# Kernel optimization log

Hardware: AMD Instinct MI355X
Metric: run time of the kernel (lower is better)

## Reference

```python
import jax, jax.numpy as jnp
import numpy as np

N, S, D = 4, 2048, 1024
H, HD = 16, 64  # heads, head_dim = patch_size // heads
SCALE = 1.0 / np.float32(np.sqrt(D))  # module divides by sqrt(patch_size), not sqrt(head_dim)


def setup_inputs() -> dict:
    key = jax.random.key(0)
    ks = jax.random.split(key, 8)
    return {
        "values": jax.random.normal(ks[0], (N, S, D), dtype=jnp.float32),
        "keys": jax.random.normal(ks[1], (N, S, D), dtype=jnp.float32),
        "query": jax.random.normal(ks[2], (N, S, D), dtype=jnp.float32),
        "Wv": jax.random.normal(ks[3], (HD, HD), dtype=jnp.float32) / np.float32(np.sqrt(HD)),
        "Wk": jax.random.normal(ks[4], (HD, HD), dtype=jnp.float32) / np.float32(np.sqrt(HD)),
        "Wq": jax.random.normal(ks[5], (HD, HD), dtype=jnp.float32) / np.float32(np.sqrt(HD)),
        "Wo": jax.random.normal(ks[6], (D, D), dtype=jnp.float32) / np.float32(np.sqrt(D)),
        "bo": jnp.zeros((D,), dtype=jnp.float32),
    }


def reference(values, keys, query, Wv, Wk, Wq, Wo, bo):
    n, ql = query.shape[0], query.shape[1]
    # reshape to heads, then per-head shared linear projections (torch Linear: x @ W.T)
    v = jnp.einsum('nlhd,ed->nlhe', values.reshape(n, -1, H, HD), Wv)
    k = jnp.einsum('nkhd,ed->nkhe', keys.reshape(n, -1, H, HD), Wk)
    q = jnp.einsum('nqhd,ed->nqhe', query.reshape(n, -1, H, HD), Wq)
    energy = jnp.einsum('nqhd,nkhd->nhqk', q, k)  # [N,H,Sq,Sk]
    attn = jax.nn.softmax(energy * SCALE, axis=3)
    out = jnp.einsum('nhql,nlhd->nqhd', attn, v).reshape(n, ql, H * HD)
    return out @ Wo.T + bo
```

## Files before the change

kernel.cpp:

```cpp
#include <hip/hip_runtime.h>
#include <stdint.h>

typedef _Float16 f16;
typedef f16 half2_t __attribute__((ext_vector_type(2)));
typedef f16 half4_t __attribute__((ext_vector_type(4)));
typedef f16 half8_t __attribute__((ext_vector_type(8)));
typedef __fp16 fp16x2_t __attribute__((ext_vector_type(2)));
typedef float f32x4 __attribute__((ext_vector_type(4)));

#define N_ 4
#define S_ 2048
#define D_ 1024
#define H_ 16
#define HD_ 64
#define LOG2E 1.44269504088896340736f
#define SCALE_ 0.03125f

typedef __attribute__((address_space(1))) void gvoid;
typedef __attribute__((address_space(3))) void lvoid;

__device__ __forceinline__ void load_lds16(const void* g, void* l) {
  __builtin_amdgcn_global_load_lds((gvoid*)(uintptr_t)g, (lvoid*)l, 16, 0, 0);
}

__device__ __forceinline__ f32x4 mfma16(half4_t a, half4_t b, f32x4 c) {
  return __builtin_amdgcn_mfma_f32_16x16x16f16(a, b, c, 0, 0, 0);
}
__device__ __forceinline__ f32x4 mfma32(half8_t a, half8_t b, f32x4 c) {
  return __builtin_amdgcn_mfma_f32_16x16x32_f16(a, b, c, 0, 0, 0);
}

__device__ __forceinline__ half2_t pack_f16(float a, float b) {
  fp16x2_t t = __builtin_amdgcn_cvt_pkrtz(a, b);
  return __builtin_bit_cast(half2_t, t);
}

#define LO4(v) __builtin_shufflevector(v, v, 0, 1, 2, 3)
#define HI4(v) __builtin_shufflevector(v, v, 4, 5, 6, 7)

__global__ void wprep(const float* __restrict__ Wv, const float* __restrict__ Wo,
                      const float* __restrict__ Wq, const float* __restrict__ Wk,
                      f16* __restrict__ Wbig, float* __restrict__ Mq) {
  int b = blockIdx.x;
  if (b < 1024) {
    int j = b;
#pragma unroll
    for (int c = 0; c < 4; ++c) {
      int i = c * 256 + threadIdx.x;
      int h = i >> 6, dd = i & 63;
      const float* wo = Wo + (size_t)j * 1024 + h * 64;
      float acc = 0.f;
#pragma unroll 8
      for (int e = 0; e < 64; ++e) acc += Wv[e * 64 + dd] * wo[e];
      Wbig[(size_t)j * 1024 + i] = (f16)acc;
    }
  } else {
    int tid = (b - 1024) * 256 + threadIdx.x;
    int d = tid >> 6, e = tid & 63;
    float acc = 0.f;
#pragma unroll 8
    for (int r = 0; r < 64; ++r) acc += Wq[r * 64 + d] * Wk[r * 64 + e];
    Mq[d * 64 + e] = acc * (SCALE_ * LOG2E);
  }
}

__global__ __launch_bounds__(256) void prep2(const float* __restrict__ Q,
                                             const float* __restrict__ K,
                                             const float* __restrict__ V,
                                             const float* __restrict__ Mq,
                                             f16* __restrict__ q16, f16* __restrict__ k16,
                                             f16* __restrict__ v16) {
  __shared__ char smem[16384];
  int b = blockIdx.x;
  if (b < 512) {
    float* mql = (float*)smem;
#pragma unroll
    for (int c = 0; c < 16; ++c) mql[c * 256 + threadIdx.x] = Mq[c * 256 + threadIdx.x];
    __syncthreads();
    int n = b >> 7, sblk = b & 127;
    int L = threadIdx.x & 63, w = threadIdx.x >> 6;
    int lq = L & 15, hh = w * 4 + (L >> 4);
    int s = sblk * 16 + lq;
    const float* qrow = Q + ((size_t)(n * S_ + s)) * D_ + hh * HD_;
    f32x4 acc4[16];
#pragma unroll
    for (int i = 0; i < 16; ++i) acc4[i] = (f32x4){0.f, 0.f, 0.f, 0.f};
    for (int d4 = 0; d4 < 16; ++d4) {
      f32x4 qv = *(const f32x4*)(qrow + d4 * 4);
#pragma unroll
      for (int dj = 0; dj < 4; ++dj) {
        const f32x4* mrow = (const f32x4*)(mql + (d4 * 4 + dj) * 64);
        float qs = qv[dj];
#pragma unroll
        for (int i = 0; i < 16; ++i) acc4[i] += mrow[i] * qs;
      }
    }
    size_t cbase = ((size_t)((n * 16 + hh) * 128 + sblk)) * 2;
#pragma unroll
    for (int dp = 0; dp < 2; ++dp) {
#pragma unroll
      for (int qd = 0; qd < 4; ++qd) {
        half8_t hv;
        f32x4 a0 = acc4[dp * 8 + qd * 2], a1 = acc4[dp * 8 + qd * 2 + 1];
#pragma unroll
        for (int j = 0; j < 4; ++j) { hv[j] = (f16)a0[j]; hv[4 + j] = (f16)a1[j]; }
        *(half8_t*)(q16 + (cbase + dp) * 512 + (qd * 16 + lq) * 8) = hv;
      }
    }
    const float* krow = K + ((size_t)(n * S_ + s)) * D_ + hh * HD_;
    f32x4 kr[16];
#pragma unroll
    for (int i = 0; i < 16; ++i) kr[i] = *(const f32x4*)(krow + i * 4);
#pragma unroll
    for (int dp = 0; dp < 2; ++dp) {
#pragma unroll
      for (int qd = 0; qd < 4; ++qd) {
        half8_t hv;
        f32x4 a0 = kr[dp * 8 + qd * 2], a1 = kr[dp * 8 + qd * 2 + 1];
#pragma unroll
        for (int j = 0; j < 4; ++j) { hv[j] = (f16)a0[j]; hv[4 + j] = (f16)a1[j]; }
        *(half8_t*)(k16 + (cbase + dp) * 512 + (qd * 16 + lq) * 8) = hv;
      }
    }
  } else {
    f16* lv = (f16*)smem;
    int b2 = b - 512;
    int n = b2 >> 10, hh = (b2 >> 6) & 15, sb = b2 & 63;
    int t = threadIdx.x;
    {
      int r = t >> 3, ic = t & 7;
      const float* src = V + ((size_t)(n * S_ + sb * 32 + r)) * D_ + hh * HD_ + ic * 8;
      f32x4 a = *(const f32x4*)src;
      f32x4 b3 = *(const f32x4*)(src + 4);
      half8_t hv;
#pragma unroll
      for (int j = 0; j < 4; ++j) { hv[j] = (f16)a[j]; hv[4 + j] = (f16)b3[j]; }
      *(half8_t*)(lv + r * 64 + ic * 8) = hv;
    }
    __syncthreads();
    {
      int mt = t >> 6, L = t & 63;
      int quad = L >> 4, ld = L & 15;
      half8_t o;
#pragma unroll
      for (int j = 0; j < 4; ++j) {
        o[j]     = lv[(quad * 4 + j) * 64 + mt * 16 + ld];
        o[4 + j] = lv[(quad * 4 + j + 16) * 64 + mt * 16 + ld];
      }
      *(half8_t*)(v16 + (((size_t)(n * 16 + hh) * 64 + sb) * 4 + mt) * 512 + L * 8) = o;
    }
  }
}

__global__ __launch_bounds__(256, 2) void flash(const f16* __restrict__ q16,
                                                const f16* __restrict__ k16,
                                                const f16* __restrict__ v16,
                                                f16* __restrict__ att) {
  __shared__ char lds[65536];
  int nh = blockIdx.x;
  int qt2 = blockIdx.y;
  int L = threadIdx.x & 63, w = threadIdx.x >> 6;
  int lq = L & 15, quad = L >> 4;

  const half8_t* qg = (const half8_t*)q16;
  half8_t qB[2][2];
#pragma unroll
  for (int j = 0; j < 2; ++j) {
    size_t qc = ((size_t)(nh * 128 + qt2 * 8 + w * 2 + j)) * 2;
    qB[j][0] = qg[qc * 64 + L];
    qB[j][1] = qg[(qc + 1) * 64 + L];
  }

  f32x4 accO[2][4];
#pragma unroll
  for (int j = 0; j < 2; ++j)
#pragma unroll
    for (int i = 0; i < 4; ++i) accO[j][i] = (f32x4){0.f, 0.f, 0.f, 0.f};
  f32x4 lvec[2] = {(f32x4){0.f, 0.f, 0.f, 0.f}, (f32x4){0.f, 0.f, 0.f, 0.f}};

  const char* kg = (const char*)k16 + (size_t)nh * 262144 + w * 4096 + L * 16;
  const char* vg = (const char*)v16 + (size_t)nh * 262144 + w * 4096 + L * 16;

#pragma unroll
  for (int t = 0; t < 2; ++t)
#pragma unroll
    for (int c = 0; c < 4; ++c) {
      load_lds16(kg + t * 16384 + c * 1024, lds + t * 16384 + w * 4096 + c * 1024);
      load_lds16(vg + t * 16384 + c * 1024, lds + 32768 + t * 16384 + w * 4096 + c * 1024);
    }
  __syncthreads();

  for (int it = 0; it < 16; ++it) {
    const char* kb = lds + (it & 1) * 16384;
    const char* vb = lds + 32768 + (it & 1) * 16384;
#pragma unroll
    for (int g = 0; g < 4; ++g) {
      half4_t pcg[2][2];
#pragma unroll
      for (int u = 0; u < 2; ++u) {
        int mt = 2 * g + u;
        half8_t k0 = *(const half8_t*)(kb + (mt * 2 + 0) * 1024 + L * 16);
        half8_t k1 = *(const half8_t*)(kb + (mt * 2 + 1) * 1024 + L * 16);
#pragma unroll
        for (int j = 0; j < 2; ++j) {
          f32x4 a = (f32x4){0.f, 0.f, 0.f, 0.f};
          a = mfma32(k0, qB[j][0], a);
          a = mfma32(k1, qB[j][1], a);
          f32x4 p;
#pragma unroll
          for (int r = 0; r < 4; ++r) p[r] = __builtin_amdgcn_exp2f(a[r]);
          lvec[j] += p;
          half2_t c01 = pack_f16(p[0], p[1]);
          half2_t c23 = pack_f16(p[2], p[3]);
          pcg[j][u] = __builtin_shufflevector(c01, c23, 0, 1, 2, 3);
        }
      }
#pragma unroll
      for (int mt2 = 0; mt2 < 4; ++mt2) {
        half8_t vf = *(const half8_t*)(vb + (g * 4 + mt2) * 1024 + L * 16);
        half4_t vlo = LO4(vf), vhi = HI4(vf);
        f32x4 a0 = accO[0][mt2], a1 = accO[1][mt2];
        a0 = mfma16(vlo, pcg[0][0], a0);
        a0 = mfma16(vhi, pcg[0][1], a0);
        a1 = mfma16(vlo, pcg[1][0], a1);
        a1 = mfma16(vhi, pcg[1][1], a1);
        accO[0][mt2] = a0; accO[1][mt2] = a1;
      }
    }
    __syncthreads();
    if (it + 2 < 16) {
      char* dk = lds + (it & 1) * 16384 + w * 4096;
      char* dv = lds + 32768 + (it & 1) * 16384 + w * 4096;
#pragma unroll
      for (int c = 0; c < 4; ++c) {
        load_lds16(kg + (size_t)(it + 2) * 16384 + c * 1024, dk + c * 1024);
        load_lds16(vg + (size_t)(it + 2) * 16384 + c * 1024, dv + c * 1024);
      }
    }
  }

  int n = nh >> 4, h = nh & 15;
#pragma unroll
  for (int j = 0; j < 2; ++j) {
    float l = lvec[j][0] + lvec[j][1] + lvec[j][2] + lvec[j][3];
    l += __shfl_xor(l, 16, 64);
    l += __shfl_xor(l, 32, 64);
    float inv_l = 1.0f / l;
    int s = qt2 * 128 + (w * 2 + j) * 16 + lq;
    f16* orow = att + ((size_t)(n * S_ + s)) * D_ + h * HD_;
#pragma unroll
    for (int mt2 = 0; mt2 < 4; ++mt2) {
      half4_t o;
#pragma unroll
      for (int r = 0; r < 4; ++r) o[r] = (f16)(accO[j][mt2][r] * inv_l);
      *(half4_t*)(orow + mt2 * 16 + quad * 4) = o;
    }
  }
}

__global__ __launch_bounds__(256, 2) void ogemm(const f16* __restrict__ A, const f16* __restrict__ Bm,
                                                const float* __restrict__ bias, float* __restrict__ C) {
  __shared__ char lds[32768];
  int bm = blockIdx.x, bn = blockIdx.y;
  int L = threadIdx.x & 63, w = threadIdx.x >> 6;
  int wm = w >> 1, wn = w & 1;
  int lq = L & 15, quad = L >> 4;
  int lr = L >> 2, lc = L & 3;
  int src_c = lc ^ (lr & 3);
  f32x4 acc[16];
#pragma unroll
  for (int i = 0; i < 16; ++i) acc[i] = (f32x4){0.f, 0.f, 0.f, 0.f};

  const f16* ga0 = A + ((size_t)(bm * 128 + (w * 2) * 16 + lr)) * 1024 + src_c * 8;
  const f16* gb0 = Bm + ((size_t)(bn * 128 + (w * 2) * 16 + lr)) * 1024 + src_c * 8;

#pragma unroll
  for (int t = 0; t < 2; ++t)
#pragma unroll
    for (int c = 0; c < 2; ++c) {
      load_lds16(ga0 + t * 32 + (size_t)c * 16 * 1024, lds + t * 16384 + (w * 2 + c) * 1024);
      load_lds16(gb0 + t * 32 + (size_t)c * 16 * 1024, lds + t * 16384 + 8192 + (w * 2 + c) * 1024);
    }
  __syncthreads();

  for (int kt = 0; kt < 32; ++kt) {
    const char* base = lds + (kt & 1) * 16384;
    half8_t af[4], bf[4];
#pragma unroll
    for (int t = 0; t < 4; ++t) {
      int ch = quad ^ (lq & 3);
      af[t] = *(const half8_t*)(base + (wm * 64 + t * 16 + lq) * 64 + ch * 16);
      bf[t] = *(const half8_t*)(base + 8192 + (wn * 64 + t * 16 + lq) * 64 + ch * 16);
    }
#pragma unroll
    for (int mt = 0; mt < 4; ++mt)
#pragma unroll
      for (int nt = 0; nt < 4; ++nt)
        acc[mt * 4 + nt] =
            __builtin_amdgcn_mfma_f32_16x16x32_f16(af[mt], bf[nt], acc[mt * 4 + nt], 0, 0, 0);
    __syncthreads();
    if (kt + 2 < 32) {
      char* dst = lds + (kt & 1) * 16384;
#pragma unroll
      for (int c = 0; c < 2; ++c) {
        load_lds16(ga0 + (kt + 2) * 32 + (size_t)c * 16 * 1024, dst + (w * 2 + c) * 1024);
        load_lds16(gb0 + (kt + 2) * 32 + (size_t)c * 16 * 1024, dst + 8192 + (w * 2 + c) * 1024);
      }
    }
  }

#pragma unroll
  for (int nt = 0; nt < 4; ++nt) {
    int col = bn * 128 + wn * 64 + nt * 16 + lq;
    float bv = bias[col];
#pragma unroll
    for (int mt = 0; mt < 4; ++mt) {
#pragma unroll
      for (int r = 0; r < 4; ++r) {
        int row = bm * 128 + wm * 64 + mt * 16 + quad * 4 + r;
        C[(size_t)row * 1024 + col] = acc[mt * 4 + nt][r] + bv;
      }
    }
  }
}

extern "C" void kernel_launch(void* const* d_in, const int* in_sizes, int n_in,
                              void* d_out, int out_size, void* d_ws, size_t ws_size,
                              hipStream_t stream) {
  const float* V  = (const float*)d_in[0];
  const float* K  = (const float*)d_in[1];
  const float* Q  = (const float*)d_in[2];
  const float* Wv = (const float*)d_in[3];
  const float* Wk = (const float*)d_in[4];
  const float* Wq = (const float*)d_in[5];
  const float* Wo = (const float*)d_in[6];
  const float* bo = (const float*)d_in[7];
  float* out = (float*)d_out;

  char* ws = (char*)d_ws;
  float* Mq  = (float*)(ws);
  f16* Wbig  = (f16*)(ws + (1ull << 20));
  f16* q16   = (f16*)(ws + (3ull << 20));
  f16* k16   = (f16*)(ws + (19ull << 20));
  f16* v16   = (f16*)(ws + (35ull << 20));
  f16* att   = (f16*)(ws + (51ull << 20));

  wprep<<<1040, 256, 0, stream>>>(Wv, Wo, Wq, Wk, Wbig, Mq);
  prep2<<<4608, 256, 0, stream>>>(Q, K, V, Mq, q16, k16, v16);
  flash<<<dim3(64, 16), 256, 0, stream>>>(q16, k16, v16, att);
  ogemm<<<dim3(64, 8), 256, 0, stream>>>(att, Wbig, bo, out);
}
```

Baseline: 290.5 us.

## Switch flash attention to 32x32x16 MFMA tiles with matching Q/K/V layouts

Reworks the attention kernel to use 32x32x16 f16 MFMA for both QK^T and PV, so each wave handles 32 query rows instead of two 16-row tiles. The prep kernel now writes Q, K and V into new fragment layouts matching the 32x32 operand format. V is transposed with strided global reads instead of through LDS. The P fragments are rebuilt in registers via cross-half lane shuffles, with no LDS round-trip. The aim is fewer MFMA issues and fewer LDS reads per FLOP, at the cost of extra shuffles, more accumulator registers, and less coalesced V loads in prep.

```diff
diff --git a/kernel.cpp b/kernel.cpp
--- a/kernel.cpp
+++ b/kernel.cpp
@@ -7,6 +7,8 @@
 typedef f16 half8_t __attribute__((ext_vector_type(8)));
 typedef __fp16 fp16x2_t __attribute__((ext_vector_type(2)));
 typedef float f32x4 __attribute__((ext_vector_type(4)));
+typedef float f32x16 __attribute__((ext_vector_type(16)));
+typedef int int4_t __attribute__((ext_vector_type(4)));
 
 #define N_ 4
 #define S_ 2048
@@ -23,20 +25,17 @@
   __builtin_amdgcn_global_load_lds((gvoid*)(uintptr_t)g, (lvoid*)l, 16, 0, 0);
 }
 
-__device__ __forceinline__ f32x4 mfma16(half4_t a, half4_t b, f32x4 c) {
-  return __builtin_amdgcn_mfma_f32_16x16x16f16(a, b, c, 0, 0, 0);
-}
-__device__ __forceinline__ f32x4 mfma32(half8_t a, half8_t b, f32x4 c) {
+__device__ __forceinline__ f32x16 mfma3216(half8_t a, half8_t b, f32x16 c) {
+  return __builtin_amdgcn_mfma_f32_32x32x16_f16(a, b, c, 0, 0, 0);
+}
+__device__ __forceinline__ f32x4 mfma1632(half8_t a, half8_t b, f32x4 c) {
   return __builtin_amdgcn_mfma_f32_16x16x32_f16(a, b, c, 0, 0, 0);
 }
 
-__device__ __forceinline__ half2_t pack_f16(float a, float b) {
+__device__ __forceinline__ int pack_f16i(float a, float b) {
   fp16x2_t t = __builtin_amdgcn_cvt_pkrtz(a, b);
-  return __builtin_bit_cast(half2_t, t);
-}
-
-#define LO4(v) __builtin_shufflevector(v, v, 0, 1, 2, 3)
-#define HI4(v) __builtin_shufflevector(v, v, 4, 5, 6, 7)
+  return __builtin_bit_cast(int, t);
+}
 
 __global__ void wprep(const float* __restrict__ Wv, const float* __restrict__ Wo,
                       const float* __restrict__ Wq, const float* __restrict__ Wk,
@@ -70,10 +69,9 @@
                                              const float* __restrict__ Mq,
                                              f16* __restrict__ q16, f16* __restrict__ k16,
                                              f16* __restrict__ v16) {
-  __shared__ char smem[16384];
+  __shared__ float mql[64 * 64];
   int b = blockIdx.x;
   if (b < 512) {
-    float* mql = (float*)smem;
 #pragma unroll
     for (int c = 0; c < 16; ++c) mql[c * 256 + threadIdx.x] = Mq[c * 256 + threadIdx.x];
     __syncthreads();
@@ -95,16 +93,17 @@
         for (int i = 0; i < 16; ++i) acc4[i] += mrow[i] * qs;
       }
     }
-    size_t cbase = ((size_t)((n * 16 + hh) * 128 + sblk)) * 2;
-#pragma unroll
-    for (int dp = 0; dp < 2; ++dp) {
-#pragma unroll
-      for (int qd = 0; qd < 4; ++qd) {
+    int nh = n * 16 + hh, sc = sblk >> 1;
+    int sh = (sblk & 1) * 16 + lq;
+#pragma unroll
+    for (int dc = 0; dc < 4; ++dc) {
+#pragma unroll
+      for (int g8 = 0; g8 < 2; ++g8) {
+        int i0 = dc * 4 + g8 * 2;
         half8_t hv;
-        f32x4 a0 = acc4[dp * 8 + qd * 2], a1 = acc4[dp * 8 + qd * 2 + 1];
-#pragma unroll
-        for (int j = 0; j < 4; ++j) { hv[j] = (f16)a0[j]; hv[4 + j] = (f16)a1[j]; }
-        *(half8_t*)(q16 + (cbase + dp) * 512 + (qd * 16 + lq) * 8) = hv;
+#pragma unroll
+        for (int j = 0; j < 4; ++j) { hv[j] = (f16)acc4[i0][j]; hv[4 + j] = (f16)acc4[i0 + 1][j]; }
+        *(half8_t*)(q16 + ((size_t)((nh * 64 + sc) * 4 + dc)) * 512 + (g8 * 32 + sh) * 8) = hv;
       }
     }
     const float* krow = K + ((size_t)(n * S_ + s)) * D_ + hh * HD_;
@@ -112,43 +111,30 @@
 #pragma unroll
     for (int i = 0; i < 16; ++i) kr[i] = *(const f32x4*)(krow + i * 4);
 #pragma unroll
-    for (int dp = 0; dp < 2; ++dp) {
-#pragma unroll
-      for (int qd = 0; qd < 4; ++qd) {
+    for (int dc = 0; dc < 4; ++dc) {
+#pragma unroll
+      for (int g8 = 0; g8 < 2; ++g8) {
+        int i0 = dc * 4 + g8 * 2;
         half8_t hv;
-        f32x4 a0 = kr[dp * 8 + qd * 2], a1 = kr[dp * 8 + qd * 2 + 1];
-#pragma unroll
-        for (int j = 0; j < 4; ++j) { hv[j] = (f16)a0[j]; hv[4 + j] = (f16)a1[j]; }
-        *(half8_t*)(k16 + (cbase + dp) * 512 + (qd * 16 + lq) * 8) = hv;
+#pragma unroll
+        for (int j = 0; j < 4; ++j) { hv[j] = (f16)kr[i0][j]; hv[4 + j] = (f16)kr[i0 + 1][j]; }
+        *(half8_t*)(k16 + ((size_t)((nh * 64 + sc) * 4 + dc)) * 512 + (g8 * 32 + sh) * 8) = hv;
       }
     }
   } else {
-    f16* lv = (f16*)smem;
-    int b2 = b - 512;
-    int n = b2 >> 10, hh = (b2 >> 6) & 15, sb = b2 & 63;
     int t = threadIdx.x;
-    {
-      int r = t >> 3, ic = t & 7;
-      const float* src = V + ((size_t)(n * S_ + sb * 32 + r)) * D_ + hh * HD_ + ic * 8;
-      f32x4 a = *(const f32x4*)src;
-      f32x4 b3 = *(const f32x4*)(src + 4);
-      half8_t hv;
-#pragma unroll
-      for (int j = 0; j < 4; ++j) { hv[j] = (f16)a[j]; hv[4 + j] = (f16)b3[j]; }
-      *(half8_t*)(lv + r * 64 + ic * 8) = hv;
-    }
-    __syncthreads();
-    {
-      int mt = t >> 6, L = t & 63;
-      int quad = L >> 4, ld = L & 15;
-      half8_t o;
-#pragma unroll
-      for (int j = 0; j < 4; ++j) {
-        o[j]     = lv[(quad * 4 + j) * 64 + mt * 16 + ld];
-        o[4 + j] = lv[(quad * 4 + j + 16) * 64 + mt * 16 + ld];
-      }
-      *(half8_t*)(v16 + (((size_t)(n * 16 + hh) * 64 + sb) * 4 + mt) * 512 + L * 8) = o;
-    }
+    int ci = (b - 512) * 4 + (t >> 6);
+    int slot = t & 63;
+    int dc32 = ci & 1, sc16 = (ci >> 1) & 127, nh = ci >> 8;
+    int n = nh >> 4, hh = nh & 15;
+    int g8 = slot >> 5, m = slot & 31;
+    int dglob = hh * 64 + dc32 * 32 + m;
+    int sbase = sc16 * 16 + g8 * 8;
+    const float* src = V + ((size_t)(n * S_ + sbase)) * D_ + dglob;
+    half8_t hv;
+#pragma unroll
+    for (int j = 0; j < 8; ++j) hv[j] = (f16)src[(size_t)j * D_];
+    *(half8_t*)(v16 + (size_t)ci * 512 + slot * 8) = hv;
   }
 }
 
@@ -160,33 +146,27 @@
   int nh = blockIdx.x;
   int qt2 = blockIdx.y;
   int L = threadIdx.x & 63, w = threadIdx.x >> 6;
-  int lq = L & 15, quad = L >> 4;
-
-  const half8_t* qg = (const half8_t*)q16;
-  half8_t qB[2][2];
-#pragma unroll
-  for (int j = 0; j < 2; ++j) {
-    size_t qc = ((size_t)(nh * 128 + qt2 * 8 + w * 2 + j)) * 2;
-    qB[j][0] = qg[qc * 64 + L];
-    qB[j][1] = qg[(qc + 1) * 64 + L];
-  }
-
-  f32x4 accO[2][4];
-#pragma unroll
-  for (int j = 0; j < 2; ++j)
-#pragma unroll
-    for (int i = 0; i < 4; ++i) accO[j][i] = (f32x4){0.f, 0.f, 0.f, 0.f};
-  f32x4 lvec[2] = {(f32x4){0.f, 0.f, 0.f, 0.f}, (f32x4){0.f, 0.f, 0.f, 0.f}};
+  int g8 = L >> 5;
+  bool hi = g8 != 0;
+
+  const f16* qptr = q16 + ((size_t)((nh * 64 + qt2 * 4 + w) * 4)) * 512 + L * 8;
+  half8_t qB[4];
+#pragma unroll
+  for (int dc = 0; dc < 4; ++dc) qB[dc] = *(const half8_t*)(qptr + dc * 512);
+
+  f32x16 acc0 = {0.f,0.f,0.f,0.f,0.f,0.f,0.f,0.f,0.f,0.f,0.f,0.f,0.f,0.f,0.f,0.f};
+  f32x16 acc1 = acc0;
+  f32x4 lvec = (f32x4){0.f, 0.f, 0.f, 0.f};
 
   const char* kg = (const char*)k16 + (size_t)nh * 262144 + w * 4096 + L * 16;
   const char* vg = (const char*)v16 + (size_t)nh * 262144 + w * 4096 + L * 16;
 
 #pragma unroll
-  for (int t = 0; t < 2; ++t)
+  for (int tt = 0; tt < 2; ++tt)
 #pragma unroll
     for (int c = 0; c < 4; ++c) {
-      load_lds16(kg + t * 16384 + c * 1024, lds + t * 16384 + w * 4096 + c * 1024);
-      load_lds16(vg + t * 16384 + c * 1024, lds + 32768 + t * 16384 + w * 4096 + c * 1024);
+      load_lds16(kg + tt * 16384 + c * 1024, lds + tt * 16384 + w * 4096 + c * 1024);
+      load_lds16(vg + tt * 16384 + c * 1024, lds + 32768 + tt * 16384 + w * 4096 + c * 1024);
     }
   __syncthreads();
 
@@ -194,37 +174,44 @@
     const char* kb = lds + (it & 1) * 16384;
     const char* vb = lds + 32768 + (it & 1) * 16384;
 #pragma unroll
-    for (int g = 0; g < 4; ++g) {
-      half4_t pcg[2][2];
-#pragma unroll
-      for (int u = 0; u < 2; ++u) {
-        int mt = 2 * g + u;
-        half8_t k0 = *(const half8_t*)(kb + (mt * 2 + 0) * 1024 + L * 16);
-        half8_t k1 = *(const half8_t*)(kb + (mt * 2 + 1) * 1024 + L * 16);
-#pragma unroll
-        for (int j = 0; j < 2; ++j) {
-          f32x4 a = (f32x4){0.f, 0.f, 0.f, 0.f};
-          a = mfma32(k0, qB[j][0], a);
-          a = mfma32(k1, qB[j][1], a);
-          f32x4 p;
-#pragma unroll
-          for (int r = 0; r < 4; ++r) p[r] = __builtin_amdgcn_exp2f(a[r]);
-          lvec[j] += p;
-          half2_t c01 = pack_f16(p[0], p[1]);
-          half2_t c23 = pack_f16(p[2], p[3]);
-          pcg[j][u] = __builtin_shufflevector(c01, c23, 0, 1, 2, 3);
-        }
-      }
-#pragma unroll
-      for (int mt2 = 0; mt2 < 4; ++mt2) {
-        half8_t vf = *(const half8_t*)(vb + (g * 4 + mt2) * 1024 + L * 16);
-        half4_t vlo = LO4(vf), vhi = HI4(vf);
-        f32x4 a0 = accO[0][mt2], a1 = accO[1][mt2];
-        a0 = mfma16(vlo, pcg[0][0], a0);
-        a0 = mfma16(vhi, pcg[0][1], a0);
-        a1 = mfma16(vlo, pcg[1][0], a1);
-        a1 = mfma16(vhi, pcg[1][1], a1);
-        accO[0][mt2] = a0; accO[1][mt2] = a1;
+    for (int c = 0; c < 4; ++c) {
+      f32x16 aS = {0.f,0.f,0.f,0.f,0.f,0.f,0.f,0.f,0.f,0.f,0.f,0.f,0.f,0.f,0.f,0.f};
+#pragma unroll
+      for (int dc = 0; dc < 4; ++dc) {
+        half8_t kf = *(const half8_t*)(kb + (c * 4 + dc) * 1024 + L * 16);
+        aS = mfma3216(kf, qB[dc], aS);
+      }
+      f32x4 pv[4];
+#pragma unroll
+      for (int r4 = 0; r4 < 4; ++r4) {
+#pragma unroll
+        for (int e = 0; e < 4; ++e) pv[r4][e] = __builtin_amdgcn_exp2f(aS[r4 * 4 + e]);
+        lvec += pv[r4];
+      }
+      int pk[8];
+#pragma unroll
+      for (int i = 0; i < 8; ++i)
+        pk[i] = pack_f16i(pv[i >> 1][(i & 1) * 2], pv[i >> 1][(i & 1) * 2 + 1]);
+      int sw[8];
+#pragma unroll
+      for (int i = 0; i < 8; ++i) sw[i] = __shfl_xor(pk[i], 32, 64);
+      half8_t fr[2];
+#pragma unroll
+      for (int sc2 = 0; sc2 < 2; ++sc2) {
+        int ba = sc2 * 4;
+        int4_t iv;
+        iv[0] = hi ? sw[ba + 2] : pk[ba + 0];
+        iv[1] = hi ? sw[ba + 3] : pk[ba + 1];
+        iv[2] = hi ? pk[ba + 2] : sw[ba + 0];
+        iv[3] = hi ? pk[ba + 3] : sw[ba + 1];
+        fr[sc2] = __builtin_bit_cast(half8_t, iv);
+      }
+#pragma unroll
+      for (int sc2 = 0; sc2 < 2; ++sc2) {
+        half8_t vf0 = *(const half8_t*)(vb + ((c * 2 + sc2) * 2 + 0) * 1024 + L * 16);
+        acc0 = mfma3216(vf0, fr[sc2], acc0);
+        half8_t vf1 = *(const half8_t*)(vb + ((c * 2 + sc2) * 2 + 1) * 1024 + L * 16);
+        acc1 = mfma3216(vf1, fr[sc2], acc1);
       }
     }
     __syncthreads();
@@ -239,21 +226,21 @@
     }
   }
 
+  float l = lvec[0] + lvec[1] + lvec[2] + lvec[3];
+  l += __shfl_xor(l, 32, 64);
+  float inv = 1.0f / l;
   int n = nh >> 4, h = nh & 15;
-#pragma unroll
-  for (int j = 0; j < 2; ++j) {
-    float l = lvec[j][0] + lvec[j][1] + lvec[j][2] + lvec[j][3];
-    l += __shfl_xor(l, 16, 64);
-    l += __shfl_xor(l, 32, 64);
-    float inv_l = 1.0f / l;
-    int s = qt2 * 128 + (w * 2 + j) * 16 + lq;
-    f16* orow = att + ((size_t)(n * S_ + s)) * D_ + h * HD_;
-#pragma unroll
-    for (int mt2 = 0; mt2 < 4; ++mt2) {
+  int s = (qt2 * 4 + w) * 32 + (L & 31);
+  f16* base = att + ((size_t)(n * S_ + s)) * D_ + h * HD_;
+#pragma unroll
+  for (int dt = 0; dt < 2; ++dt) {
+    f32x16 A = dt ? acc1 : acc0;
+#pragma unroll
+    for (int blk = 0; blk < 4; ++blk) {
       half4_t o;
 #pragma unroll
-      for (int r = 0; r < 4; ++r) o[r] = (f16)(accO[j][mt2][r] * inv_l);
-      *(half4_t*)(orow + mt2 * 16 + quad * 4) = o;
+      for (int r = 0; r < 4; ++r) o[r] = (f16)(A[blk * 4 + r] * inv);
+      *(half4_t*)(base + dt * 32 + blk * 8 + g8 * 4) = o;
     }
   }
 }
@@ -296,8 +283,7 @@
     for (int mt = 0; mt < 4; ++mt)
 #pragma unroll
       for (int nt = 0; nt < 4; ++nt)
-        acc[mt * 4 + nt] =
-            __builtin_amdgcn_mfma_f32_16x16x32_f16(af[mt], bf[nt], acc[mt * 4 + nt], 0, 0, 0);
+        acc[mt * 4 + nt] = mfma1632(af[mt], bf[nt], acc[mt * 4 + nt]);
     __syncthreads();
     if (kt + 2 < 32) {
       char* dst = lds + (kt & 1) * 16384;
```

Measured after the change: 291.5 us. About the same (+0.3%).
